# Kernel tuning notes

Hardware: AMD Instinct MI355X
Metric: run time of the kernel (lower is better)

Reference implementation:

```python
import jax, jax.numpy as jnp
import numpy as np

NUM_HEADS = 8      # SD1.x UNet cross-attn heads at 64x64 block
NUM_PROMPTS = 4    # batch = 2*NUM_PROMPTS (uncond + cond CFG halves)


def setup_inputs() -> dict:
    key = jax.random.key(0)
    ks = jax.random.split(key, 8)
    B, T, C = 2 * NUM_PROMPTS, 4096, 320   # spatial tokens, inner dim
    S, D = 77, 768                          # CLIP text seq len / width
    return {
        "hidden_states": jax.random.normal(ks[0], (B, T, C), jnp.float32),
        "encoder_hidden_states": jax.random.normal(ks[1], (B, S, D), jnp.float32),
        "mapper": jax.random.uniform(ks[2], (NUM_PROMPTS - 1, S, S), jnp.float32),
        "Wq": jax.random.normal(ks[3], (C, C), jnp.float32) * 0.02,
        "Wk": jax.random.normal(ks[4], (D, C), jnp.float32) * 0.02,
        "Wv": jax.random.normal(ks[5], (D, C), jnp.float32) * 0.02,
        "Wo": jax.random.normal(ks[6], (C, C), jnp.float32) * 0.02,
        "bo": jnp.zeros((C,), jnp.float32),
    }


def reference(hidden_states, encoder_hidden_states, mapper, Wq, Wk, Wv, Wo, bo):
    B, T, C = hidden_states.shape
    S = encoder_hidden_states.shape[1]
    H = NUM_HEADS
    d = C // H
    scale = 1.0 / jnp.sqrt(jnp.asarray(d, hidden_states.dtype))

    # projections + head split (diffusers head_to_batch_dim layout)
    q = (hidden_states @ Wq).reshape(B, T, H, d)
    k = (encoder_hidden_states @ Wk).reshape(B, S, H, d)
    v = (encoder_hidden_states @ Wv).reshape(B, S, H, d)

    # full attention probabilities must be materialized for the P2P swap
    scores = jnp.einsum('bthd,bshd->bhts', q, k) * scale
    probs = jax.nn.softmax(scores, axis=-1)  # [B, H, T, S]

    # conditional (CFG) half: [P, H, T, S]; swap via mapper einsum (cross-attn,
    # cur_step < num_steps_cross branch of swap_attention_probs)
    half = B // 2
    uncond = probs[:half]
    cond = probs[half:]
    attn_base = cond[0]                                   # [H, T, S]
    replaced = jnp.einsum('htm,pme->phte', attn_base, mapper)  # [P-1, H, T, S]
    cond = jnp.concatenate([attn_base[None], replaced], axis=0)
    probs = jnp.concatenate([uncond, cond], axis=0)

    # value matmul + merge heads (batch_to_head_dim) + output projection
    out = jnp.einsum('bhts,bshd->bthd', probs, v).reshape(B, T, C)
    return out @ Wo + bo
```

## Files before the change

kernel.cpp:

```cpp
#include <hip/hip_runtime.h>
#include <hip/hip_bf16.h>

typedef unsigned short ushort;
typedef __attribute__((ext_vector_type(8))) short bf16x8;
typedef __attribute__((ext_vector_type(8))) unsigned short ushort8;
typedef __attribute__((ext_vector_type(4))) float f32x4;
typedef __attribute__((ext_vector_type(4))) float float4v;

__device__ __forceinline__ ushort f2bf(float f) {
    union { float f; unsigned u; } v; v.f = f;
    unsigned r = v.u + 0x7FFFu + ((v.u >> 16) & 1u);
    return (ushort)(r >> 16);
}
__device__ __forceinline__ float bf2f(ushort u) {
    union { unsigned u; float f; } v; v.u = ((unsigned)u) << 16;
    return v.f;
}

#define QF_SZ   (1280u * 8 * 2 * 512)
#define KF_SZ   (5u * 8 * 5 * 2 * 512)
#define VF_SZ   (5u * 8 * 3 * 3 * 512)
#define VPF_SZ  (3u * 8 * 3 * 3 * 512)

__global__ __launch_bounds__(256) void zero_fill(
    ushort* __restrict__ Kf, ushort* __restrict__ Vf, ushort* __restrict__ VPf)
{
    const ushort8 z8 = {0,0,0,0,0,0,0,0};
    unsigned i = blockIdx.x * 256 + threadIdx.x;
    if (i < KF_SZ / 8) ((ushort8*)Kf)[i] = z8;
    else if (i < (KF_SZ + VF_SZ) / 8) ((ushort8*)Vf)[i - KF_SZ / 8] = z8;
    else if (i < (KF_SZ + VF_SZ + VPF_SZ) / 8) ((ushort8*)VPf)[i - (KF_SZ + VF_SZ) / 8] = z8;
}

__global__ __launch_bounds__(256) void transpose_all(
    const float* __restrict__ Wq, const float* __restrict__ Wk,
    const float* __restrict__ Wv, const float* __restrict__ Wo,
    ushort* __restrict__ Wq_t, ushort* __restrict__ Wk_t,
    ushort* __restrict__ Wv_t, ushort* __restrict__ Wo_t)
{
    __shared__ ushort t[32][33];
    int b = blockIdx.x;
    const float* src; ushort* dst; int K; int tb;
    if (b < 100)      { src = Wq; dst = Wq_t; K = 320; tb = b; }
    else if (b < 340) { src = Wk; dst = Wk_t; K = 768; tb = b - 100; }
    else if (b < 580) { src = Wv; dst = Wv_t; K = 768; tb = b - 340; }
    else              { src = Wo; dst = Wo_t; K = 320; tb = b - 580; }
    int tc = tb % 10, tr = tb / 10;
    int tx = threadIdx.x & 31, ty = threadIdx.x >> 5;
    #pragma unroll
    for (int p = 0; p < 4; ++p) {
        int k = tr * 32 + ty + p * 8, n = tc * 32 + tx;
        t[ty + p * 8][tx] = f2bf(src[(size_t)k * 320 + n]);
    }
    __syncthreads();
    #pragma unroll
    for (int p = 0; p < 4; ++p) {
        int n = tc * 32 + ty + p * 8, k = tr * 32 + tx;
        dst[(size_t)n * K + k] = t[tx][ty + p * 8];
    }
}

__global__ __launch_bounds__(256) void gemm_qkv(
    const float* __restrict__ A, const ushort* __restrict__ Wq_t,
    const float* __restrict__ E, const ushort* __restrict__ Wk_t,
    const ushort* __restrict__ Wv_t,
    ushort* __restrict__ Qf, float* __restrict__ part)
{
    __shared__ ushort A_lds[2][64 * 40];
    __shared__ ushort B_lds[2][320 * 40];
    const int tid = threadIdx.x;
    const int w = tid >> 6, l = tid & 63;
    const int c15 = l & 15, khi = (l >> 4) * 8;
    const int r = tid >> 2, p = (tid & 3) * 8;
    const int rbase = (l >> 4) * 4;
    f32x4 acc[4][5] = {};
    const int bid = blockIdx.x;
    const ushort8 z8 = {0,0,0,0,0,0,0,0};

    if (bid < 160) {
        const int mtile = bid % 10, mat = (bid / 10) & 1, ks = bid / 20;
        const int m0 = mtile * 64, kk0 = ks * 96;
        const ushort* Bt = mat ? Wv_t : Wk_t;
        const int m = m0 + r;
        const bool live = (m < 616);
        const float* Abase = E + (size_t)(live ? m : 0) * 768 + p;
        float4v a0 = {0,0,0,0}, a1 = {0,0,0,0};
        ushort8 breg[5];
        if (live) { a0 = *(const float4v*)(Abase + kk0); a1 = *(const float4v*)(Abase + kk0 + 4); }
        #pragma unroll
        for (int i = 0; i < 5; ++i) {
            int idx = tid + i * 256; int n = idx >> 2, q = (idx & 3) * 8;
            breg[i] = *(const ushort8*)(Bt + (size_t)n * 768 + kk0 + q);
        }
        {
            ushort* d = &A_lds[0][r * 40 + p];
            d[0]=f2bf(a0.x); d[1]=f2bf(a0.y); d[2]=f2bf(a0.z); d[3]=f2bf(a0.w);
            d[4]=f2bf(a1.x); d[5]=f2bf(a1.y); d[6]=f2bf(a1.z); d[7]=f2bf(a1.w);
            #pragma unroll
            for (int i = 0; i < 5; ++i) {
                int idx = tid + i * 256; int n = idx >> 2, q = (idx & 3) * 8;
                *(ushort8*)&B_lds[0][n * 40 + q] = breg[i];
            }
        }
        __syncthreads();
        for (int k = 0; k < 3; ++k) {
            const int cur = k & 1;
            if (k < 2) {
                int kk = kk0 + (k + 1) * 32;
                if (live) { a0 = *(const float4v*)(Abase + kk); a1 = *(const float4v*)(Abase + kk + 4); }
                #pragma unroll
                for (int i = 0; i < 5; ++i) {
                    int idx = tid + i * 256; int n = idx >> 2, q = (idx & 3) * 8;
                    breg[i] = *(const ushort8*)(Bt + (size_t)n * 768 + kk + q);
                }
            }
            bf16x8 a[4];
            #pragma unroll
            for (int mf = 0; mf < 4; ++mf)
                a[mf] = *(const bf16x8*)&A_lds[cur][(mf * 16 + c15) * 40 + khi];
            #pragma unroll
            for (int f = 0; f < 5; ++f) {
                bf16x8 b = *(const bf16x8*)&B_lds[cur][(w * 80 + f * 16 + c15) * 40 + khi];
                #pragma unroll
                for (int mf = 0; mf < 4; ++mf)
                    acc[mf][f] = __builtin_amdgcn_mfma_f32_16x16x32_bf16(a[mf], b, acc[mf][f], 0, 0, 0);
            }
            if (k < 2) {
                const int nxt = cur ^ 1;
                ushort* d = &A_lds[nxt][r * 40 + p];
                d[0]=f2bf(a0.x); d[1]=f2bf(a0.y); d[2]=f2bf(a0.z); d[3]=f2bf(a0.w);
                d[4]=f2bf(a1.x); d[5]=f2bf(a1.y); d[6]=f2bf(a1.z); d[7]=f2bf(a1.w);
                #pragma unroll
                for (int i = 0; i < 5; ++i) {
                    int idx = tid + i * 256; int n = idx >> 2, q = (idx & 3) * 8;
                    *(ushort8*)&B_lds[nxt][n * 40 + q] = breg[i];
                }
                __syncthreads();
            }
        }
        float* dst = part + (size_t)(mat * 8 + ks) * 640 * 320;
        #pragma unroll
        for (int mf = 0; mf < 4; ++mf)
            #pragma unroll
            for (int f = 0; f < 5; ++f) {
                int col = w * 80 + f * 16 + c15;
                #pragma unroll
                for (int rr = 0; rr < 4; ++rr)
                    dst[(size_t)(m0 + mf * 16 + rbase + rr) * 320 + col] = acc[mf][f][rr];
            }
    } else {
        const int m0 = (bid - 160) * 64;
        const float* Abase = A + (size_t)(m0 + r) * 320 + p;
        float4v a0, a1; ushort8 breg[5];
        a0 = *(const float4v*)(Abase + 0);
        a1 = *(const float4v*)(Abase + 4);
        #pragma unroll
        for (int i = 0; i < 5; ++i) {
            int idx = tid + i * 256; int n = idx >> 2, q = (idx & 3) * 8;
            breg[i] = *(const ushort8*)(Wq_t + (size_t)n * 320 + q);
        }
        {
            ushort* d = &A_lds[0][r * 40 + p];
            d[0]=f2bf(a0.x); d[1]=f2bf(a0.y); d[2]=f2bf(a0.z); d[3]=f2bf(a0.w);
            d[4]=f2bf(a1.x); d[5]=f2bf(a1.y); d[6]=f2bf(a1.z); d[7]=f2bf(a1.w);
            #pragma unroll
            for (int i = 0; i < 5; ++i) {
                int idx = tid + i * 256; int n = idx >> 2, q = (idx & 3) * 8;
                *(ushort8*)&B_lds[0][n * 40 + q] = breg[i];
            }
        }
        __syncthreads();
        for (int k = 0; k < 10; ++k) {
            const int cur = k & 1;
            if (k < 9) {
                int kk = (k + 1) * 32;
                a0 = *(const float4v*)(Abase + kk);
                a1 = *(const float4v*)(Abase + kk + 4);
                #pragma unroll
                for (int i = 0; i < 5; ++i) {
                    int idx = tid + i * 256; int n = idx >> 2, q = (idx & 3) * 8;
                    breg[i] = *(const ushort8*)(Wq_t + (size_t)n * 320 + kk + q);
                }
            }
            bf16x8 a[4];
            #pragma unroll
            for (int mf = 0; mf < 4; ++mf)
                a[mf] = *(const bf16x8*)&A_lds[cur][(mf * 16 + c15) * 40 + khi];
            #pragma unroll
            for (int f = 0; f < 5; ++f) {
                bf16x8 b = *(const bf16x8*)&B_lds[cur][(w * 80 + f * 16 + c15) * 40 + khi];
                #pragma unroll
                for (int mf = 0; mf < 4; ++mf)
                    acc[mf][f] = __builtin_amdgcn_mfma_f32_16x16x32_bf16(a[mf], b, acc[mf][f], 0, 0, 0);
            }
            if (k < 9) {
                const int nxt = cur ^ 1;
                ushort* d = &A_lds[nxt][r * 40 + p];
                d[0]=f2bf(a0.x); d[1]=f2bf(a0.y); d[2]=f2bf(a0.z); d[3]=f2bf(a0.w);
                d[4]=f2bf(a1.x); d[5]=f2bf(a1.y); d[6]=f2bf(a1.z); d[7]=f2bf(a1.w);
                #pragma unroll
                for (int i = 0; i < 5; ++i) {
                    int idx = tid + i * 256; int n = idx >> 2, q = (idx & 3) * 8;
                    *(ushort8*)&B_lds[nxt][n * 40 + q] = breg[i];
                }
                __syncthreads();
            }
        }
        const int rg0 = m0 >> 4;
        for (int i = tid; i < 1536; i += 256) {
            int grp = i / 48;
            int lane16 = 16 + (i - grp * 48);
            int rg4 = grp >> 3, h = grp & 7;
            *(ushort8*)(Qf + ((size_t)((rg0 + rg4) * 8 + h) * 2 + 1) * 512 + lane16 * 8) = z8;
        }
        #pragma unroll
        for (int mf = 0; mf < 4; ++mf)
            #pragma unroll
            for (int f = 0; f < 5; ++f) {
                int col = w * 80 + f * 16 + c15;
                int h = col / 40, kd = col - h * 40;
                int kt = kd >> 5, chunk = (kd >> 3) & 3, elem = kd & 7;
                size_t base = ((size_t)((rg0 + mf) * 8 + h) * 2 + kt) * 512;
                #pragma unroll
                for (int rr = 0; rr < 4; ++rr) {
                    int lane = (rbase + rr) | (chunk << 4);
                    Qf[base + lane * 8 + elem] = f2bf(acc[mf][f][rr]);
                }
            }
    }
}

__global__ __launch_bounds__(256) void kv_reduce(
    const float* __restrict__ part, ushort* __restrict__ Kf,
    ushort* __restrict__ Vf, ushort* __restrict__ VVt)
{
    int idx = blockIdx.x * 256 + threadIdx.x;
    if (idx >= 616 * 320) return;
    int mat = blockIdx.y;
    int row = idx / 320, col = idx - row * 320;
    float s8 = 0.f;
    #pragma unroll
    for (int ks = 0; ks < 8; ++ks)
        s8 += part[((size_t)(mat * 8 + ks) * 640 + row) * 320 + col];
    ushort b = f2bf(s8);
    int bt = row / 77, s = row - bt * 77;
    int h = col / 40, kd = col - h * 40;
    if (mat == 0) {
        if (bt < 5) {
            int kt = kd >> 5, chunk = (kd >> 3) & 3;
            int lane = (s & 15) | (chunk << 4);
            Kf[((size_t)((bt * 8 + h) * 5 + (s >> 4)) * 2 + kt) * 512 + lane * 8 + (kd & 7)] = b;
        }
    } else {
        if (bt < 5) {
            int lane = (kd & 15) | (((s >> 3) & 3) << 4);
            Vf[(((size_t)(bt * 8 + h) * 3 + (kd >> 4)) * 3 + (s >> 5)) * 512 + lane * 8 + (s & 7)] = b;
        } else {
            VVt[((size_t)bt * 320 + col) * 80 + s] = b;
        }
    }
}

__global__ void vprime_k(const float* __restrict__ mapper, const ushort* __restrict__ VVt,
                         ushort* __restrict__ VPf)
{
    int pm = blockIdx.x;
    int p = pm / 77, m = pm - p * 77;
    __shared__ float mp[77];
    int tid = threadIdx.x;
    if (tid < 77) mp[tid] = mapper[(size_t)pm * 77 + tid];
    __syncthreads();
    const ushort* vrow = VVt + ((size_t)(5 + p) * 320 + tid) * 80;
    float acc = 0.f;
    for (int e = 0; e < 77; ++e) acc += mp[e] * bf2f(vrow[e]);
    int h = tid / 40, dc = tid - h * 40;
    int lane = (dc & 15) | (((m >> 3) & 3) << 4);
    VPf[(((size_t)(p * 8 + h) * 3 + (dc >> 4)) * 3 + (m >> 5)) * 512 + lane * 8 + (m & 7)] = f2bf(acc);
}

#define ATT_SCALE 0.15811388300841897f
__global__ __launch_bounds__(512, 4) void attn_out_k(
    const ushort* __restrict__ Qf, const ushort* __restrict__ Kf,
    const ushort* __restrict__ Vf, const ushort* __restrict__ VPf,
    const ushort* __restrict__ Wo_t, const float* __restrict__ bias,
    float* __restrict__ out)
{
    __shared__ __align__(16) ushort AO_lds[64 * 328];
    __shared__ __align__(16) ushort P_lds[8 * 16 * 104];
    ushort* W_lds = P_lds;

    const int tid = threadIdx.x;
    const int ww = tid >> 6, l = tid & 63;
    const int rg = ww & 3, half = ww >> 2;
    const int c15 = l & 15, hi4 = l >> 4;
    const int khi = hi4 * 8, rbase = hi4 * 4;
    const int bt = blockIdx.y, t0 = blockIdx.x * 64;
    const int qb = (bt < 5) ? bt : 4;
    const int rowgrp = qb * 256 + blockIdx.x * 4 + rg;
    const ushort* Vfb = (bt < 5) ? (Vf + (size_t)bt * (8 * 3 * 3 * 512))
                                 : (VPf + (size_t)(bt - 5) * (8 * 3 * 3 * 512));
    const ushort8 z8 = {0,0,0,0,0,0,0,0};
    ushort* Pw = P_lds + ww * (16 * 104);

    if (l < 48) {
        int r = l / 3, c = l - 3 * (l / 3);
        *(ushort8*)&Pw[r * 104 + 80 + c * 8] = z8;
    }

    for (int hh = 0; hh < 4; ++hh) {
        const int h = half * 4 + hh;

        bf16x8 qa0 = *(const bf16x8*)(Qf + ((size_t)(rowgrp * 8 + h) * 2 + 0) * 512 + l * 8);
        bf16x8 qa1 = *(const bf16x8*)(Qf + ((size_t)(rowgrp * 8 + h) * 2 + 1) * 512 + l * 8);
        f32x4 sacc[5] = {};
        #pragma unroll
        for (int f = 0; f < 5; ++f) {
            const ushort* kfb = Kf + ((size_t)((qb * 8 + h) * 5 + f) * 2) * 512 + l * 8;
            bf16x8 kb0 = *(const bf16x8*)(kfb);
            bf16x8 kb1 = *(const bf16x8*)(kfb + 512);
            sacc[f] = __builtin_amdgcn_mfma_f32_16x16x32_bf16(qa0, kb0, sacc[f], 0, 0, 0);
            sacc[f] = __builtin_amdgcn_mfma_f32_16x16x32_bf16(qa1, kb1, sacc[f], 0, 0, 0);
        }

        bf16x8 vreg[3][3];
        #pragma unroll
        for (int f = 0; f < 3; ++f)
            #pragma unroll
            for (int kt = 0; kt < 3; ++kt)
                vreg[f][kt] = *(const bf16x8*)(Vfb + (((size_t)(h * 3 + f) * 3 + kt)) * 512 + l * 8);

        float pv[5][4];
        #pragma unroll
        for (int r = 0; r < 4; ++r) {
            float sum = 0.f;
            #pragma unroll
            for (int f = 0; f < 5; ++f) {
                bool valid = (f < 4) || (c15 < 13);
                float e = valid ? __expf(sacc[f][r] * ATT_SCALE) : 0.f;
                pv[f][r] = e; sum += e;
            }
            #pragma unroll
            for (int d = 1; d < 16; d <<= 1) sum += __shfl_xor(sum, d);
            float inv = 1.f / sum;
            #pragma unroll
            for (int f = 0; f < 5; ++f) pv[f][r] *= inv;
        }

        #pragma unroll
        for (int r = 0; r < 4; ++r)
            #pragma unroll
            for (int f = 0; f < 5; ++f)
                Pw[(rbase + r) * 104 + f * 16 + c15] = f2bf(pv[f][r]);

        bf16x8 pa[3];
        #pragma unroll
        for (int kt = 0; kt < 3; ++kt)
            pa[kt] = *(const bf16x8*)&Pw[c15 * 104 + kt * 32 + khi];
        f32x4 oacc[3] = {};
        #pragma unroll
        for (int f = 0; f < 3; ++f)
            #pragma unroll
            for (int kt = 0; kt < 3; ++kt)
                oacc[f] = __builtin_amdgcn_mfma_f32_16x16x32_bf16(pa[kt], vreg[f][kt], oacc[f], 0, 0, 0);
        #pragma unroll
        for (int f = 0; f < 3; ++f) {
            int col = f * 16 + c15;
            if (col < 40) {
                #pragma unroll
                for (int r = 0; r < 4; ++r)
                    AO_lds[(rg * 16 + rbase + r) * 328 + h * 40 + col] = f2bf(oacc[f][r]);
            }
        }
    }
    __syncthreads();

    const int cb = half * 160;
    f32x4 acc[10] = {};
    for (int kk = 0; kk < 10; ++kk) {
        if (kk) __syncthreads();
        #pragma unroll
        for (int i = 0; i < 3; ++i) {
            int idx = tid + i * 512;
            if (idx < 1280) {
                int n = idx >> 2, c = idx & 3;
                *(ushort8*)&W_lds[n * 40 + c * 8] =
                    *(const ushort8*)(Wo_t + (size_t)n * 320 + kk * 32 + c * 8);
            }
        }
        __syncthreads();
        bf16x8 a = *(const bf16x8*)&AO_lds[(rg * 16 + c15) * 328 + kk * 32 + khi];
        #pragma unroll
        for (int f = 0; f < 10; ++f) {
            bf16x8 b = *(const bf16x8*)&W_lds[(cb + f * 16 + c15) * 40 + khi];
            acc[f] = __builtin_amdgcn_mfma_f32_16x16x32_bf16(a, b, acc[f], 0, 0, 0);
        }
    }

    #pragma unroll
    for (int f = 0; f < 10; ++f) {
        int col = cb + f * 16 + c15;
        #pragma unroll
        for (int rr = 0; rr < 4; ++rr)
            out[(size_t)(bt * 4096 + t0 + rg * 16 + rbase + rr) * 320 + col]
                = acc[f][rr] + bias[col];
    }
}

extern "C" void kernel_launch(void* const* d_in, const int* in_sizes, int n_in,
                              void* d_out, int out_size, void* d_ws, size_t ws_size,
                              hipStream_t stream) {
    (void)in_sizes; (void)n_in; (void)out_size; (void)ws_size;
    const float* hs     = (const float*)d_in[0];
    const float* ehs    = (const float*)d_in[1];
    const float* mapper = (const float*)d_in[2];
    const float* Wq     = (const float*)d_in[3];
    const float* Wk     = (const float*)d_in[4];
    const float* Wv     = (const float*)d_in[5];
    const float* Wo     = (const float*)d_in[6];
    const float* bo     = (const float*)d_in[7];
    float* out = (float*)d_out;

    ushort* ws   = (ushort*)d_ws;
    ushort* Wq_t = ws;
    ushort* Wk_t = Wq_t + 320 * 320;
    ushort* Wv_t = Wk_t + 320 * 768;
    ushort* Wo_t = Wv_t + 320 * 768;
    ushort* Qfb  = Wo_t + 320 * 320;
    ushort* Kfb  = Qfb + QF_SZ;
    ushort* Vfb  = Kfb + KF_SZ;
    ushort* VPfb = Vfb + VF_SZ;
    ushort* VVt  = VPfb + VPF_SZ;
    float*  part = (float*)(VVt + 8 * 320 * 80);

    zero_fill<<<389, 256, 0, stream>>>(Kfb, Vfb, VPfb);
    transpose_all<<<680, 256, 0, stream>>>(Wq, Wk, Wv, Wo, Wq_t, Wk_t, Wv_t, Wo_t);
    gemm_qkv<<<480, 256, 0, stream>>>(hs, Wq_t, ehs, Wk_t, Wv_t, Qfb, part);
    kv_reduce<<<dim3(770, 2), 256, 0, stream>>>(part, Kfb, Vfb, VVt);
    vprime_k<<<231, 320, 0, stream>>>(mapper, VVt, VPfb);
    attn_out_k<<<dim3(64, 8), 512, 0, stream>>>(Qfb, Kfb, Vfb, VPfb, Wo_t, bo, out);
}
```

Baseline: 73.42 us.

## Prepack Wo into MFMA fragment layout and merge zero-fill into transpose kernel

Wo_t is now repacked into a per-lane MFMA B-fragment layout by extra blocks added to gemm_qkv. The output projection in attn_out_k then loads B operands straight from global memory instead of staging them through LDS with two barriers per k-step. Separately, the zero-fill kernel is folded into the weight transpose kernel as extra blocks, removing one launch. The trade-off is that each wave now reads its Wo fragments from global or L2 directly, where before they were shared through LDS, and a small extra workspace buffer is used.

Result: faster. 68.54 us (-6.6%).

```diff
diff --git a/kernel.cpp b/kernel.cpp
--- a/kernel.cpp
+++ b/kernel.cpp
@@ -21,25 +21,25 @@
 #define KF_SZ   (5u * 8 * 5 * 2 * 512)
 #define VF_SZ   (5u * 8 * 3 * 3 * 512)
 #define VPF_SZ  (3u * 8 * 3 * 3 * 512)
-
-__global__ __launch_bounds__(256) void zero_fill(
-    ushort* __restrict__ Kf, ushort* __restrict__ Vf, ushort* __restrict__ VPf)
-{
-    const ushort8 z8 = {0,0,0,0,0,0,0,0};
-    unsigned i = blockIdx.x * 256 + threadIdx.x;
-    if (i < KF_SZ / 8) ((ushort8*)Kf)[i] = z8;
-    else if (i < (KF_SZ + VF_SZ) / 8) ((ushort8*)Vf)[i - KF_SZ / 8] = z8;
-    else if (i < (KF_SZ + VF_SZ + VPF_SZ) / 8) ((ushort8*)VPf)[i - (KF_SZ + VF_SZ) / 8] = z8;
-}
-
-__global__ __launch_bounds__(256) void transpose_all(
+#define WOF_SZ  (10u * 2 * 10 * 512)
+
+__global__ __launch_bounds__(256) void prep_k(
     const float* __restrict__ Wq, const float* __restrict__ Wk,
     const float* __restrict__ Wv, const float* __restrict__ Wo,
     ushort* __restrict__ Wq_t, ushort* __restrict__ Wk_t,
-    ushort* __restrict__ Wv_t, ushort* __restrict__ Wo_t)
+    ushort* __restrict__ Wv_t, ushort* __restrict__ Wo_t,
+    ushort* __restrict__ Kf, ushort* __restrict__ Vf, ushort* __restrict__ VPf)
 {
+    int b = blockIdx.x;
+    if (b >= 680) {
+        const ushort8 z8 = {0,0,0,0,0,0,0,0};
+        unsigned i = (b - 680) * 256 + threadIdx.x;
+        if (i < KF_SZ / 8) ((ushort8*)Kf)[i] = z8;
+        else if (i < (KF_SZ + VF_SZ) / 8) ((ushort8*)Vf)[i - KF_SZ / 8] = z8;
+        else if (i < (KF_SZ + VF_SZ + VPF_SZ) / 8) ((ushort8*)VPf)[i - (KF_SZ + VF_SZ) / 8] = z8;
+        return;
+    }
     __shared__ ushort t[32][33];
-    int b = blockIdx.x;
     const float* src; ushort* dst; int K; int tb;
     if (b < 100)      { src = Wq; dst = Wq_t; K = 320; tb = b; }
     else if (b < 340) { src = Wk; dst = Wk_t; K = 768; tb = b - 100; }
@@ -63,18 +63,28 @@
 __global__ __launch_bounds__(256) void gemm_qkv(
     const float* __restrict__ A, const ushort* __restrict__ Wq_t,
     const float* __restrict__ E, const ushort* __restrict__ Wk_t,
-    const ushort* __restrict__ Wv_t,
-    ushort* __restrict__ Qf, float* __restrict__ part)
+    const ushort* __restrict__ Wv_t, const ushort* __restrict__ Wo_t,
+    ushort* __restrict__ Qf, float* __restrict__ part, ushort* __restrict__ Wof)
 {
+    const int tid = threadIdx.x;
+    const int bid = blockIdx.x;
+    if (bid >= 480) {
+        int i = (bid - 480) * 256 + tid;
+        int g = i >> 6, l = i & 63;
+        int kk = g / 20, half = (g / 10) & 1, f = g - (g / 10) * 10;
+        int n = half * 160 + f * 16 + (l & 15);
+        int k0 = kk * 32 + (l >> 4) * 8;
+        *(ushort8*)(Wof + (size_t)g * 512 + l * 8) =
+            *(const ushort8*)(Wo_t + (size_t)n * 320 + k0);
+        return;
+    }
     __shared__ ushort A_lds[2][64 * 40];
     __shared__ ushort B_lds[2][320 * 40];
-    const int tid = threadIdx.x;
     const int w = tid >> 6, l = tid & 63;
     const int c15 = l & 15, khi = (l >> 4) * 8;
     const int r = tid >> 2, p = (tid & 3) * 8;
     const int rbase = (l >> 4) * 4;
     f32x4 acc[4][5] = {};
-    const int bid = blockIdx.x;
     const ushort8 z8 = {0,0,0,0,0,0,0,0};
 
     if (bid < 160) {
@@ -282,12 +292,11 @@
 __global__ __launch_bounds__(512, 4) void attn_out_k(
     const ushort* __restrict__ Qf, const ushort* __restrict__ Kf,
     const ushort* __restrict__ Vf, const ushort* __restrict__ VPf,
-    const ushort* __restrict__ Wo_t, const float* __restrict__ bias,
+    const ushort* __restrict__ Wof, const float* __restrict__ bias,
     float* __restrict__ out)
 {
     __shared__ __align__(16) ushort AO_lds[64 * 328];
     __shared__ __align__(16) ushort P_lds[8 * 16 * 104];
-    ushort* W_lds = P_lds;
 
     const int tid = threadIdx.x;
     const int ww = tid >> 6, l = tid & 63;
@@ -374,28 +383,18 @@
     }
     __syncthreads();
 
-    const int cb = half * 160;
     f32x4 acc[10] = {};
     for (int kk = 0; kk < 10; ++kk) {
-        if (kk) __syncthreads();
-        #pragma unroll
-        for (int i = 0; i < 3; ++i) {
-            int idx = tid + i * 512;
-            if (idx < 1280) {
-                int n = idx >> 2, c = idx & 3;
-                *(ushort8*)&W_lds[n * 40 + c * 8] =
-                    *(const ushort8*)(Wo_t + (size_t)n * 320 + kk * 32 + c * 8);
-            }
-        }
-        __syncthreads();
         bf16x8 a = *(const bf16x8*)&AO_lds[(rg * 16 + c15) * 328 + kk * 32 + khi];
+        const ushort* wb = Wof + (size_t)((kk * 2 + half) * 10) * 512 + l * 8;
         #pragma unroll
         for (int f = 0; f < 10; ++f) {
-            bf16x8 b = *(const bf16x8*)&W_lds[(cb + f * 16 + c15) * 40 + khi];
+            bf16x8 b = *(const bf16x8*)(wb + (size_t)f * 512);
             acc[f] = __builtin_amdgcn_mfma_f32_16x16x32_bf16(a, b, acc[f], 0, 0, 0);
         }
     }
 
+    const int cb = half * 160;
     #pragma unroll
     for (int f = 0; f < 10; ++f) {
         int col = cb + f * 16 + c15;
@@ -425,17 +424,18 @@
     ushort* Wk_t = Wq_t + 320 * 320;
     ushort* Wv_t = Wk_t + 320 * 768;
     ushort* Wo_t = Wv_t + 320 * 768;
-    ushort* Qfb  = Wo_t + 320 * 320;
+    ushort* Wof  = Wo_t + 320 * 320;
+    ushort* Qfb  = Wof + WOF_SZ;
     ushort* Kfb  = Qfb + QF_SZ;
     ushort* Vfb  = Kfb + KF_SZ;
     ushort* VPfb = Vfb + VF_SZ;
     ushort* VVt  = VPfb + VPF_SZ;
     float*  part = (float*)(VVt + 8 * 320 * 80);
 
-    zero_fill<<<389, 256, 0, stream>>>(Kfb, Vfb, VPfb);
-    transpose_all<<<680, 256, 0, stream>>>(Wq, Wk, Wv, Wo, Wq_t, Wk_t, Wv_t, Wo_t);
-    gemm_qkv<<<480, 256, 0, stream>>>(hs, Wq_t, ehs, Wk_t, Wv_t, Qfb, part);
+    prep_k<<<1069, 256, 0, stream>>>(Wq, Wk, Wv, Wo, Wq_t, Wk_t, Wv_t, Wo_t,
+                                     Kfb, Vfb, VPfb);
+    gemm_qkv<<<530, 256, 0, stream>>>(hs, Wq_t, ehs, Wk_t, Wv_t, Wo_t, Qfb, part, Wof);
     kv_reduce<<<dim3(770, 2), 256, 0, stream>>>(part, Kfb, Vfb, VVt);
     vprime_k<<<231, 320, 0, stream>>>(mapper, VVt, VPfb);
-    attn_out_k<<<dim3(64, 8), 512, 0, stream>>>(Qfb, Kfb, Vfb, VPfb, Wo_t, bo, out);
-}
+    attn_out_k<<<dim3(64, 8), 512, 0, stream>>>(Qfb, Kfb, Vfb, VPfb, Wof, bo, out);
+}
```
